# Kernel optimization log

Hardware: AMD Instinct MI355X
Metric: run time of the kernel (lower is better)

The kernel has to match this reference:

```python
import jax, jax.numpy as jnp
import numpy as np

N_NODES = 100000
N_EDGES = 1600000
D_IN = 128
D_HID = 128
N_CLASSES = 4
N_GRAPHS = 512


def setup_inputs() -> dict:
    key = jax.random.key(0)
    ks = jax.random.split(key, 10)
    x = jax.random.normal(ks[0], (N_NODES, D_IN), dtype=jnp.float32)
    edge_index = jax.random.randint(ks[1], (2, N_EDGES), 0, N_NODES, dtype=jnp.int64)
    batch = jnp.sort(jax.random.randint(ks[2], (N_NODES,), 0, N_GRAPHS, dtype=jnp.int64))
    s = 1.0 / np.sqrt(D_IN)
    W1l = jax.random.uniform(ks[3], (D_HID, D_IN), jnp.float32, -s, s)
    W1r = jax.random.uniform(ks[4], (D_HID, D_IN), jnp.float32, -s, s)
    b1 = jnp.zeros((D_HID,), jnp.float32)
    s2 = 1.0 / np.sqrt(D_HID)
    W2l = jax.random.uniform(ks[5], (D_HID, D_HID), jnp.float32, -s2, s2)
    W2r = jax.random.uniform(ks[6], (D_HID, D_HID), jnp.float32, -s2, s2)
    b2 = jnp.zeros((D_HID,), jnp.float32)
    Wlin = jax.random.uniform(ks[7], (N_CLASSES, D_HID), jnp.float32, -s2, s2)
    blin = jax.random.uniform(ks[8], (N_CLASSES,), jnp.float32, -s2, s2)
    return {"x": x, "edge_index": edge_index, "batch": batch,
            "W1l": W1l, "b1": b1, "W1r": W1r,
            "W2l": W2l, "b2": b2, "W2r": W2r,
            "Wlin": Wlin, "blin": blin}


def _sage_conv(x, src, dst, deg_inv, W_l, b, W_r):
    # mean-aggregate neighbor features (messages flow src -> dst)
    agg = jax.ops.segment_sum(x[src], dst, num_segments=N_NODES) * deg_inv
    return agg @ W_l.T + b + x @ W_r.T


def reference(x, edge_index, batch, W1l, b1, W1r, W2l, b2, W2r, Wlin, blin):
    src, dst = edge_index[0], edge_index[1]
    ones = jnp.ones((src.shape[0],), x.dtype)
    deg = jax.ops.segment_sum(ones, dst, num_segments=N_NODES)
    deg_inv = (1.0 / jnp.maximum(deg, 1.0))[:, None]

    h = jax.nn.relu(_sage_conv(x, src, dst, deg_inv, W1l, b1, W1r))
    h = jax.nn.relu(_sage_conv(h, src, dst, deg_inv, W2l, b2, W2r))

    # global mean pool over graphs
    gsum = jax.ops.segment_sum(h, batch, num_segments=N_GRAPHS)
    gcnt = jax.ops.segment_sum(jnp.ones((N_NODES,), h.dtype), batch, num_segments=N_GRAPHS)
    pooled = gsum / jnp.maximum(gcnt, 1.0)[:, None]

    # dropout is identity in eval mode
    return pooled @ Wlin.T + blin
```

## Files before the change

kernel.cpp:

```cpp
#include <hip/hip_runtime.h>
#include <hip/hip_bf16.h>


#define NN 100000
#define NE 1600000
#define DH 128
#define NG 512
#define CSTRIDE 48
#define NBKT 8
#define BKT_SZ 12500
#define NSLICE 100
#define ESLICE 16000
#define NFILL 800
#define NPREP 6250

#define PSUM_SCALE  1048576.0f
#define PSUM_INV    (1.0f/1048576.0f)

typedef __hip_bfloat16 bf16;
typedef __bf16 bf16x8 __attribute__((ext_vector_type(8)));
typedef float  f32x4  __attribute__((ext_vector_type(4)));
typedef float  f32x2  __attribute__((ext_vector_type(2)));
typedef int    i32x4  __attribute__((ext_vector_type(4)));
typedef unsigned u32x2 __attribute__((ext_vector_type(2)));
typedef unsigned u32x4 __attribute__((ext_vector_type(4)));
typedef unsigned char u8;

__device__ __forceinline__ void bf8_to_f(uint4 q, float* w) {
    union { unsigned u; float f; } t;
    t.u = q.x << 16;          w[0] = t.f;
    t.u = q.x & 0xffff0000u;  w[1] = t.f;
    t.u = q.y << 16;          w[2] = t.f;
    t.u = q.y & 0xffff0000u;  w[3] = t.f;
    t.u = q.z << 16;          w[4] = t.f;
    t.u = q.z & 0xffff0000u;  w[5] = t.f;
    t.u = q.w << 16;          w[6] = t.f;
    t.u = q.w & 0xffff0000u;  w[7] = t.f;
}

__device__ __forceinline__ unsigned pack4_fp8(float a, float b, float c, float d) {
    int p = __builtin_amdgcn_cvt_pk_fp8_f32(a, b, 0, false);
    p = __builtin_amdgcn_cvt_pk_fp8_f32(c, d, p, true);
    return (unsigned)p;
}


__global__ __launch_bounds__(256) void k_fill_prep(
    const int* __restrict__ ei, int* __restrict__ deg, int* __restrict__ col,
    const float* __restrict__ x, u8* __restrict__ fq,
    const float* __restrict__ w0, const float* __restrict__ w1,
    const float* __restrict__ w2, const float* __restrict__ w3,
    bf16* __restrict__ wb,
    const int* __restrict__ batch, int* __restrict__ cnt)
{
    const int bid = blockIdx.x, tid = threadIdx.x;

    if (bid < NFILL) {
        const int bucket = bid & (NBKT - 1);
        const int wi     = bid >> 3;
        const int lo = bucket * BKT_SZ, hi = lo + BKT_SZ;
        const int e0 = wi * ESLICE;
        const i32x4* dp = (const i32x4*)(ei + NE + e0);
        const i32x4* sp = (const i32x4*)(ei + e0);
        for (int v = tid; v < ESLICE / 4; v += 256) {
            i32x4 d4 = __builtin_nontemporal_load(dp + v);
            bool m0 = d4[0] >= lo && d4[0] < hi;
            bool m1 = d4[1] >= lo && d4[1] < hi;
            bool m2 = d4[2] >= lo && d4[2] < hi;
            bool m3 = d4[3] >= lo && d4[3] < hi;
            if (m0 | m1 | m2 | m3) {
                i32x4 s4 = __builtin_nontemporal_load(sp + v);
                if (m0) { int p = atomicAdd(&deg[d4[0]], 1); if (p < CSTRIDE) col[d4[0] * CSTRIDE + p] = s4[0]; }
                if (m1) { int p = atomicAdd(&deg[d4[1]], 1); if (p < CSTRIDE) col[d4[1] * CSTRIDE + p] = s4[1]; }
                if (m2) { int p = atomicAdd(&deg[d4[2]], 1); if (p < CSTRIDE) col[d4[2] * CSTRIDE + p] = s4[2]; }
                if (m3) { int p = atomicAdd(&deg[d4[3]], 1); if (p < CSTRIDE) col[d4[3] * CSTRIDE + p] = s4[3]; }
            }
        }
        return;
    }

    const int pb = bid - NFILL;
    {
        int g = pb * 256 + tid;
        const f32x4* s = (const f32x4*)(x + (size_t)g * 8);
        f32x4 u0 = __builtin_nontemporal_load(s);
        f32x4 u1 = __builtin_nontemporal_load(s + 1);
        u32x2 v;
        v[0] = pack4_fp8(u0[0], u0[1], u0[2], u0[3]);
        v[1] = pack4_fp8(u1[0], u1[1], u1[2], u1[3]);
        __builtin_nontemporal_store(v, (u32x2*)(fq + (size_t)g * 8));
    }
    if (pb < 256) {
        int gid = pb * 256 + tid;
        int m = gid >> 14, i = gid & 16383;
        const float* src = (m == 0) ? w0 : (m == 1) ? w1 : (m == 2) ? w2 : w3;
        wb[gid] = __float2bfloat16(src[i]);
    } else if (pb < 258) {
        int g = (pb - 256) * 256 + tid;
        if (g < NG) {
            int lo0 = 0, hi0 = NN, lo1 = 0, hi1 = NN;
            while (lo0 < hi0) { int m = (lo0 + hi0) >> 1; if (batch[m] < g)     lo0 = m + 1; else hi0 = m; }
            while (lo1 < hi1) { int m = (lo1 + hi1) >> 1; if (batch[m] < g + 1) lo1 = m + 1; else hi1 = m; }
            cnt[g] = lo1 - lo0;
        }
    }
}


__global__ __launch_bounds__(256) void k_gather(
    const int* __restrict__ deg, const int* __restrict__ col,
    const u8* __restrict__ fq, bf16* __restrict__ agg)
{
    const int nid  = blockIdx.x * 4 + (threadIdx.x >> 6);
    const int lane = threadIdx.x & 63;
    const int qsub = lane >> 4;
    const int l4   = lane & 15;
    int dgr = __builtin_amdgcn_readfirstlane(deg[nid]);
    int dg = dgr > CSTRIDE ? CSTRIDE : dgr;
    int vidx = (lane < CSTRIDE) ? col[nid * CSTRIDE + lane] : 0;

    float a[8] = {0.f, 0.f, 0.f, 0.f, 0.f, 0.f, 0.f, 0.f};

    for (int e = 0; e < dg; e += 8) {
        int sa0 = __builtin_amdgcn_readlane(vidx, min(e + 0, dg - 1));
        int sa1 = __builtin_amdgcn_readlane(vidx, min(e + 1, dg - 1));
        int sa2 = __builtin_amdgcn_readlane(vidx, min(e + 2, dg - 1));
        int sa3 = __builtin_amdgcn_readlane(vidx, min(e + 3, dg - 1));
        int sb0 = __builtin_amdgcn_readlane(vidx, min(e + 4, dg - 1));
        int sb1 = __builtin_amdgcn_readlane(vidx, min(e + 5, dg - 1));
        int sb2 = __builtin_amdgcn_readlane(vidx, min(e + 6, dg - 1));
        int sb3 = __builtin_amdgcn_readlane(vidx, min(e + 7, dg - 1));
        int sA = (qsub == 0) ? sa0 : (qsub == 1) ? sa1 : (qsub == 2) ? sa2 : sa3;
        int sB = (qsub == 0) ? sb0 : (qsub == 1) ? sb1 : (qsub == 2) ? sb2 : sb3;
        float mA = (e + qsub     < dg) ? 1.f : 0.f;
        float mB = (e + 4 + qsub < dg) ? 1.f : 0.f;
        uint2 qA = *(const uint2*)(fq + (size_t)sA * DH + l4 * 8);
        uint2 qB = *(const uint2*)(fq + (size_t)sB * DH + l4 * 8);
        f32x2 v0 = __builtin_amdgcn_cvt_pk_f32_fp8((int)qA.x, false);
        f32x2 v1 = __builtin_amdgcn_cvt_pk_f32_fp8((int)qA.x, true);
        f32x2 v2 = __builtin_amdgcn_cvt_pk_f32_fp8((int)qA.y, false);
        f32x2 v3 = __builtin_amdgcn_cvt_pk_f32_fp8((int)qA.y, true);
        a[0] += v0[0] * mA; a[1] += v0[1] * mA;
        a[2] += v1[0] * mA; a[3] += v1[1] * mA;
        a[4] += v2[0] * mA; a[5] += v2[1] * mA;
        a[6] += v3[0] * mA; a[7] += v3[1] * mA;
        v0 = __builtin_amdgcn_cvt_pk_f32_fp8((int)qB.x, false);
        v1 = __builtin_amdgcn_cvt_pk_f32_fp8((int)qB.x, true);
        v2 = __builtin_amdgcn_cvt_pk_f32_fp8((int)qB.y, false);
        v3 = __builtin_amdgcn_cvt_pk_f32_fp8((int)qB.y, true);
        a[0] += v0[0] * mB; a[1] += v0[1] * mB;
        a[2] += v1[0] * mB; a[3] += v1[1] * mB;
        a[4] += v2[0] * mB; a[5] += v2[1] * mB;
        a[6] += v3[0] * mB; a[7] += v3[1] * mB;
    }

    #pragma unroll
    for (int i = 0; i < 8; ++i) {
        a[i] += __shfl_xor(a[i], 16, 64);
        a[i] += __shfl_xor(a[i], 32, 64);
    }

    if (qsub == 0) {
        float di = 1.0f / fmaxf((float)dgr, 1.0f);
        union { bf16 b[8]; u32x4 u; } pk;
        #pragma unroll
        for (int i = 0; i < 8; ++i) pk.b[i] = __float2bfloat16(a[i] * di);
        __builtin_nontemporal_store(pk.u, (u32x4*)(agg + nid * DH + l4 * 8));
    }
}


#define WSTR 136

template <bool POOL>
__global__ __launch_bounds__(256, 4) void k_layer(
    const bf16* __restrict__ agg, const u8* __restrict__ xq,
    const bf16* __restrict__ Wlb, const bf16* __restrict__ Wrb,
    const float* __restrict__ bias,
    u8* __restrict__ outq, int* __restrict__ psum,
    const int* __restrict__ batch)
{
    __shared__ bf16 wl[128 * WSTR];
    __shared__ int  bb[128];

    const int tid  = threadIdx.x;
    const int wave = tid >> 6;
    const int lane = tid & 63;
    const int lm   = lane & 15;
    const int kg   = lane >> 4;
    const int base = blockIdx.x * 128;
    const int wbase = base + wave * 32;

    const int r0 = min(wbase + lm,      NN - 1);
    const int r1 = min(wbase + 16 + lm, NN - 1);

    if (POOL && tid < 128) bb[tid] = batch[min(base + tid, NN - 1)];

    {
        const int row = tid >> 1, half = tid & 1;
        const uint4* src = (const uint4*)(Wlb + row * DH + half * 64);
        uint4* dst = (uint4*)(wl + row * WSTR + half * 64);
        #pragma unroll
        for (int i = 0; i < 8; ++i) dst[i] = src[i];
    }
    __syncthreads();

    f32x4 acc[2][8];
    #pragma unroll
    for (int i = 0; i < 2; ++i)
        #pragma unroll
        for (int t = 0; t < 8; ++t)
            acc[i][t] = (f32x4){0.f, 0.f, 0.f, 0.f};

    #pragma unroll
    for (int kc = 0; kc < 4; ++kc) {
        const int ko = kc * 32 + kg * 8;
        bf16x8 a0 = *(const bf16x8*)(agg + r0 * DH + ko);
        bf16x8 a1 = *(const bf16x8*)(agg + r1 * DH + ko);
        #pragma unroll
        for (int t = 0; t < 8; ++t) {
            bf16x8 b = *(const bf16x8*)(wl + (t * 16 + lm) * WSTR + ko);
            acc[0][t] = __builtin_amdgcn_mfma_f32_16x16x32_bf16(a0, b, acc[0][t], 0, 0, 0);
            acc[1][t] = __builtin_amdgcn_mfma_f32_16x16x32_bf16(a1, b, acc[1][t], 0, 0, 0);
        }
    }
    __syncthreads();

    {
        const int row = tid >> 1, half = tid & 1;
        const uint4* src = (const uint4*)(Wrb + row * DH + half * 64);
        uint4* dst = (uint4*)(wl + row * WSTR + half * 64);
        #pragma unroll
        for (int i = 0; i < 8; ++i) dst[i] = src[i];
    }
    __syncthreads();

    #pragma unroll
    for (int kc = 0; kc < 4; ++kc) {
        const int ko = kc * 32 + kg * 8;
        bf16x8 a0, a1;
        uint2 q0 = *(const uint2*)(xq + (size_t)r0 * DH + ko);
        uint2 q1 = *(const uint2*)(xq + (size_t)r1 * DH + ko);
        f32x2 c0 = __builtin_amdgcn_cvt_pk_f32_fp8((int)q0.x, false);
        f32x2 c1 = __builtin_amdgcn_cvt_pk_f32_fp8((int)q0.x, true);
        f32x2 c2 = __builtin_amdgcn_cvt_pk_f32_fp8((int)q0.y, false);
        f32x2 c3 = __builtin_amdgcn_cvt_pk_f32_fp8((int)q0.y, true);
        a0[0] = (__bf16)c0[0]; a0[1] = (__bf16)c0[1];
        a0[2] = (__bf16)c1[0]; a0[3] = (__bf16)c1[1];
        a0[4] = (__bf16)c2[0]; a0[5] = (__bf16)c2[1];
        a0[6] = (__bf16)c3[0]; a0[7] = (__bf16)c3[1];
        c0 = __builtin_amdgcn_cvt_pk_f32_fp8((int)q1.x, false);
        c1 = __builtin_amdgcn_cvt_pk_f32_fp8((int)q1.x, true);
        c2 = __builtin_amdgcn_cvt_pk_f32_fp8((int)q1.y, false);
        c3 = __builtin_amdgcn_cvt_pk_f32_fp8((int)q1.y, true);
        a1[0] = (__bf16)c0[0]; a1[1] = (__bf16)c0[1];
        a1[2] = (__bf16)c1[0]; a1[3] = (__bf16)c1[1];
        a1[4] = (__bf16)c2[0]; a1[5] = (__bf16)c2[1];
        a1[6] = (__bf16)c3[0]; a1[7] = (__bf16)c3[1];
        #pragma unroll
        for (int t = 0; t < 8; ++t) {
            bf16x8 b = *(const bf16x8*)(wl + (t * 16 + lm) * WSTR + ko);
            acc[0][t] = __builtin_amdgcn_mfma_f32_16x16x32_bf16(a0, b, acc[0][t], 0, 0, 0);
            acc[1][t] = __builtin_amdgcn_mfma_f32_16x16x32_bf16(a1, b, acc[1][t], 0, 0, 0);
        }
    }
    __syncthreads();

    bf16* ob = wl;
    const int quad = lane >> 4;
    #pragma unroll
    for (int i = 0; i < 2; ++i) {
        #pragma unroll
        for (int r = 0; r < 4; ++r) {
            const int lr = wave * 32 + i * 16 + quad * 4 + r;
            const int n  = base + lr;
            #pragma unroll
            for (int t = 0; t < 8; ++t) {
                const int f = t * 16 + lm;
                float v = fmaxf(acc[i][t][r] + bias[f], 0.f);
                if (POOL && n >= NN) v = 0.f;
                ob[lr * DH + f] = __float2bfloat16(v);
            }
        }
    }
    __syncthreads();

    if (!POOL) {
        uint2* d = (uint2*)(outq + (size_t)base * DH);
        #pragma unroll
        for (int i = 0; i < 8; ++i) {
            const int idx = i * 256 + tid;
            const int n = base + (idx >> 4);
            if (n < NN) {
                uint4 s = ((const uint4*)ob)[idx];
                float w[8];
                bf8_to_f(s, w);
                uint2 o;
                o.x = pack4_fp8(w[0], w[1], w[2], w[3]);
                o.y = pack4_fp8(w[4], w[5], w[6], w[7]);
                d[idx] = o;
            }
        }
    } else {
        const int f = tid & 127, h = tid >> 7;
        float rs = 0.f;
        int cur = bb[h * 64];
        #pragma unroll 8
        for (int r = 0; r < 64; ++r) {
            const int row = h * 64 + r;
            float v = __bfloat162float(ob[row * DH + f]);
            int b = bb[row];
            if (b != cur) {
                atomicAdd(&psum[cur * DH + f], __float2int_rn(rs * PSUM_SCALE));
                rs = 0.f; cur = b;
            }
            rs += v;
        }
        atomicAdd(&psum[cur * DH + f], __float2int_rn(rs * PSUM_SCALE));
    }
}


__global__ __launch_bounds__(256) void k_final(
    const int* __restrict__ psum, const int* __restrict__ cnt,
    const float* __restrict__ Wlin, const float* __restrict__ blin,
    float* __restrict__ out)
{
    int gid = blockIdx.x * 256 + threadIdx.x;
    if (gid >= NG * 4) return;
    int gph = gid >> 2, c = gid & 3;
    const int* p = psum + gph * DH;
    const float* w = Wlin + c * DH;
    float s = 0.f;
    #pragma unroll 8
    for (int k = 0; k < DH; ++k)
        s += (float)p[k] * w[k];
    float inv = 1.0f / fmaxf((float)cnt[gph], 1.0f);
    out[gid] = s * PSUM_INV * inv + blin[c];
}

extern "C" void kernel_launch(void* const* d_in, const int* in_sizes, int n_in,
                              void* d_out, int out_size, void* d_ws, size_t ws_size,
                              hipStream_t stream) {
    const float* x     = (const float*)d_in[0];
    const int*   ei    = (const int*)d_in[1];
    const int*   batch = (const int*)d_in[2];
    const float* W1l   = (const float*)d_in[3];
    const float* b1    = (const float*)d_in[4];
    const float* W1r   = (const float*)d_in[5];
    const float* W2l   = (const float*)d_in[6];
    const float* b2    = (const float*)d_in[7];
    const float* W2r   = (const float*)d_in[8];
    const float* Wlin  = (const float*)d_in[9];
    const float* blin  = (const float*)d_in[10];
    float* out = (float*)d_out;

    char* base = (char*)d_ws;
    int*   deg  = (int*)(base + 64);
    int*   cnt  = (int*)(base + 400064);
    int*   psum = (int*)(base + 402112);
    bf16*  wb   = (bf16*)(base + 664256);
    int*   col  = (int*)(base + 795328);
    bf16*  agg  = (bf16*)(base + 19995328);
    u8*    fq   = (u8*)(base + 45595328);

    bf16* W1lb = wb;
    bf16* W1rb = wb + 16384;
    bf16* W2lb = wb + 32768;
    bf16* W2rb = wb + 49152;

    hipMemsetAsync(d_ws, 0, 664256, stream);

    k_fill_prep<<<NFILL + NPREP, 256, 0, stream>>>(
        ei, deg, col, x, fq, W1l, W1r, W2l, W2r, wb, batch, cnt);

    k_gather<<<NN / 4, 256, 0, stream>>>(deg, col, fq, agg);
    k_layer<false><<<(NN + 127) / 128, 256, 0, stream>>>(agg, fq, W1lb, W1rb, b1,
                                                         fq, nullptr, nullptr);

    k_gather<<<NN / 4, 256, 0, stream>>>(deg, col, fq, agg);
    k_layer<true><<<(NN + 127) / 128, 256, 0, stream>>>(agg, fq, W2lb, W2rb, b2,
                                                        nullptr, psum, batch);

    k_final<<<8, 256, 0, stream>>>(psum, cnt, Wlin, blin, out);
}
```

Measured before the change: 340.3 us.

## Replace global-atomic CSR fill with counting-sort bucketing and LDS-atomic fill

Adjacency construction moves from many blocks rescanning all edges and doing global atomics per destination to a three-pass counting sort. The first pass builds per-slice histograms over 49 destination sub-buckets alongside the existing prep work. The second pass scatters packed (dst, src) pairs into bucket order. The third pass fills the column lists using shared-memory degree counters, which also removes the need to zero deg with a memset. In exchange it adds two kernel launches, an extra 12.8MB intermediate buffer that is written then read, heavily contended LDS atomics on only 49 counters, and a final pass limited to 49 blocks.

```diff
diff --git a/kernel.cpp b/kernel.cpp
--- a/kernel.cpp
+++ b/kernel.cpp
@@ -7,12 +7,12 @@
 #define DH 128
 #define NG 512
 #define CSTRIDE 48
-#define NBKT 8
-#define BKT_SZ 12500
-#define NSLICE 100
-#define ESLICE 16000
-#define NFILL 800
 #define NPREP 6250
+
+#define NSUB 49
+#define SUBSH 11
+#define NSCAN 256
+#define ESPS 6250
 
 #define PSUM_SCALE  1048576.0f
 #define PSUM_INV    (1.0f/1048576.0f)
@@ -21,10 +21,10 @@
 typedef __bf16 bf16x8 __attribute__((ext_vector_type(8)));
 typedef float  f32x4  __attribute__((ext_vector_type(4)));
 typedef float  f32x2  __attribute__((ext_vector_type(2)));
-typedef int    i32x4  __attribute__((ext_vector_type(4)));
 typedef unsigned u32x2 __attribute__((ext_vector_type(2)));
 typedef unsigned u32x4 __attribute__((ext_vector_type(4)));
 typedef unsigned char u8;
+typedef unsigned long long u64;
 
 __device__ __forceinline__ void bf8_to_f(uint4 q, float* w) {
     union { unsigned u; float f; } t;
@@ -45,8 +45,8 @@
 }
 
 
-__global__ __launch_bounds__(256) void k_fill_prep(
-    const int* __restrict__ ei, int* __restrict__ deg, int* __restrict__ col,
+__global__ __launch_bounds__(256) void k_prep(
+    const int* __restrict__ ei, int* __restrict__ ccnt,
     const float* __restrict__ x, u8* __restrict__ fq,
     const float* __restrict__ w0, const float* __restrict__ w1,
     const float* __restrict__ w2, const float* __restrict__ w3,
@@ -55,31 +55,21 @@
 {
     const int bid = blockIdx.x, tid = threadIdx.x;
 
-    if (bid < NFILL) {
-        const int bucket = bid & (NBKT - 1);
-        const int wi     = bid >> 3;
-        const int lo = bucket * BKT_SZ, hi = lo + BKT_SZ;
-        const int e0 = wi * ESLICE;
-        const i32x4* dp = (const i32x4*)(ei + NE + e0);
-        const i32x4* sp = (const i32x4*)(ei + e0);
-        for (int v = tid; v < ESLICE / 4; v += 256) {
-            i32x4 d4 = __builtin_nontemporal_load(dp + v);
-            bool m0 = d4[0] >= lo && d4[0] < hi;
-            bool m1 = d4[1] >= lo && d4[1] < hi;
-            bool m2 = d4[2] >= lo && d4[2] < hi;
-            bool m3 = d4[3] >= lo && d4[3] < hi;
-            if (m0 | m1 | m2 | m3) {
-                i32x4 s4 = __builtin_nontemporal_load(sp + v);
-                if (m0) { int p = atomicAdd(&deg[d4[0]], 1); if (p < CSTRIDE) col[d4[0] * CSTRIDE + p] = s4[0]; }
-                if (m1) { int p = atomicAdd(&deg[d4[1]], 1); if (p < CSTRIDE) col[d4[1] * CSTRIDE + p] = s4[1]; }
-                if (m2) { int p = atomicAdd(&deg[d4[2]], 1); if (p < CSTRIDE) col[d4[2] * CSTRIDE + p] = s4[2]; }
-                if (m3) { int p = atomicAdd(&deg[d4[3]], 1); if (p < CSTRIDE) col[d4[3] * CSTRIDE + p] = s4[3]; }
-            }
-        }
+    if (bid < NSCAN) {
+        __shared__ int c[NSUB];
+        if (tid < NSUB) c[tid] = 0;
+        __syncthreads();
+        const int e0 = bid * ESPS;
+        for (int e = e0 + tid; e < e0 + ESPS; e += 256) {
+            int d = __builtin_nontemporal_load(ei + NE + e);
+            atomicAdd(&c[d >> SUBSH], 1);
+        }
+        __syncthreads();
+        if (tid < NSUB) ccnt[tid * NSCAN + bid] = c[tid];
         return;
     }
 
-    const int pb = bid - NFILL;
+    const int pb = bid - NSCAN;
     {
         int g = pb * 256 + tid;
         const f32x4* s = (const f32x4*)(x + (size_t)g * 8);
@@ -103,6 +93,76 @@
             while (lo1 < hi1) { int m = (lo1 + hi1) >> 1; if (batch[m] < g + 1) lo1 = m + 1; else hi1 = m; }
             cnt[g] = lo1 - lo0;
         }
+    }
+}
+
+
+__global__ __launch_bounds__(256) void k_scatter(
+    const int* __restrict__ ei, const int* __restrict__ ccnt,
+    u64* __restrict__ pe, int* __restrict__ bkb)
+{
+    const int s = blockIdx.x, tid = threadIdx.x;
+    __shared__ int rank[NSUB];
+    __shared__ int lbase[NSUB];
+
+    if (tid < NSUB) {
+        int pref = 0, tot = 0;
+        const int* row = ccnt + tid * NSCAN;
+        for (int s2 = 0; s2 < NSCAN; ++s2) {
+            int c = row[s2];
+            if (s2 < s) pref += c;
+            tot += c;
+        }
+        lbase[tid] = tot;
+        rank[tid]  = pref;
+    }
+    __syncthreads();
+    if (tid == 0) {
+        int run = 0;
+        for (int g = 0; g < NSUB; ++g) { int t = lbase[g]; lbase[g] = run; run += t; }
+    }
+    __syncthreads();
+    if (tid < NSUB) {
+        rank[tid] += lbase[tid];
+        if (s == 0) bkb[tid] = lbase[tid];
+    }
+    __syncthreads();
+
+    const int e0 = s * ESPS;
+    for (int e = e0 + tid; e < e0 + ESPS; e += 256) {
+        int d   = __builtin_nontemporal_load(ei + NE + e);
+        int src = __builtin_nontemporal_load(ei + e);
+        int g = d >> SUBSH;
+        int pos = atomicAdd(&rank[g], 1);
+        pe[pos] = ((u64)(unsigned)d << 32) | (unsigned)src;
+    }
+}
+
+
+__global__ __launch_bounds__(256) void k_fill2(
+    const u64* __restrict__ pe, const int* __restrict__ bkb,
+    int* __restrict__ deg, int* __restrict__ col)
+{
+    const int g = blockIdx.x, tid = threadIdx.x;
+    __shared__ int degL[1 << SUBSH];
+    for (int i = tid; i < (1 << SUBSH); i += 256) degL[i] = 0;
+    __syncthreads();
+
+    const int lo = bkb[g];
+    const int hi = (g == NSUB - 1) ? NE : bkb[g + 1];
+    const int nb = g << SUBSH;
+    for (int e = lo + tid; e < hi; e += 256) {
+        u64 p = pe[e];
+        int d   = (int)(p >> 32);
+        int src = (int)(p & 0xffffffffu);
+        int pos = atomicAdd(&degL[d - nb], 1);
+        if (pos < CSTRIDE) col[d * CSTRIDE + pos] = src;
+    }
+    __syncthreads();
+
+    for (int i = tid; i < (1 << SUBSH); i += 256) {
+        int n = nb + i;
+        if (n < NN) deg[n] = degL[i];
     }
 }
 
@@ -360,19 +420,24 @@
     int*   cnt  = (int*)(base + 400064);
     int*   psum = (int*)(base + 402112);
     bf16*  wb   = (bf16*)(base + 664256);
-    int*   col  = (int*)(base + 795328);
-    bf16*  agg  = (bf16*)(base + 19995328);
-    u8*    fq   = (u8*)(base + 45595328);
+    int*   ccnt = (int*)(base + 795328);
+    int*   bkb  = (int*)(base + 845504);
+    int*   col  = (int*)(base + 845760);
+    bf16*  agg  = (bf16*)(base + 20045760);
+    u8*    fq   = (u8*)(base + 45645760);
+    u64*   pe   = (u64*)(base + 58445760);
 
     bf16* W1lb = wb;
     bf16* W1rb = wb + 16384;
     bf16* W2lb = wb + 32768;
     bf16* W2rb = wb + 49152;
 
-    hipMemsetAsync(d_ws, 0, 664256, stream);
-
-    k_fill_prep<<<NFILL + NPREP, 256, 0, stream>>>(
-        ei, deg, col, x, fq, W1l, W1r, W2l, W2r, wb, batch, cnt);
+    hipMemsetAsync(base + 402112, 0, 262144, stream);
+
+    k_prep<<<NSCAN + NPREP, 256, 0, stream>>>(
+        ei, ccnt, x, fq, W1l, W1r, W2l, W2r, wb, batch, cnt);
+    k_scatter<<<NSCAN, 256, 0, stream>>>(ei, ccnt, pe, bkb);
+    k_fill2<<<NSUB, 256, 0, stream>>>(pe, bkb, deg, col);
 
     k_gather<<<NN / 4, 256, 0, stream>>>(deg, col, fq, agg);
     k_layer<false><<<(NN + 127) / 128, 256, 0, stream>>>(agg, fq, W1lb, W1rb, b1,
```

Result: slower. 357.3 us (+5.0%).
